# Kernel tuning notes

Measured on AMD Instinct MI355X. Metric: run time of the kernel, lower is better.

## Reference

```python
import jax, jax.numpy as jnp
import numpy as np

H = 8          # num_heads
D = 64         # out_dims = input_dims / num_heads
DM = H * D     # input_dims = 512
B, S = 2, 2048


def _linear(x, W, b):
    # torch nn.Linear: x @ W.T + b, W: [out, in]
    return jnp.einsum('...d,ed->...e', x, W) + b


def setup_inputs() -> dict:
    key = jax.random.key(0)
    ks = jax.random.split(key, 12)
    inp = {
        'query': jax.random.normal(ks[0], (B, S, DM), dtype=jnp.float32),
        'key': jax.random.normal(ks[1], (B, S, DM), dtype=jnp.float32),
        'value': jax.random.normal(ks[2], (B, S, DM), dtype=jnp.float32),
        'Wq': jax.random.normal(ks[3], (D, D), dtype=jnp.float32) * 0.02,
        'bq': jnp.zeros((D,), dtype=jnp.float32),
        'Wk': jax.random.normal(ks[4], (D, D), dtype=jnp.float32) * 0.02,
        'bk': jnp.zeros((D,), dtype=jnp.float32),
        'Wv': jax.random.normal(ks[5], (D, D), dtype=jnp.float32) * 0.02,
        'bv': jnp.zeros((D,), dtype=jnp.float32),
        'Wo': jax.random.normal(ks[6], (DM, DM), dtype=jnp.float32) * 0.02,
        'bo': jnp.zeros((DM,), dtype=jnp.float32),
        'mask': jax.random.randint(ks[7], (B, 1, 1, S), 0, 2, dtype=jnp.int32),
    }
    return inp


def reference(query, key, value, Wq, bq, Wk, bk, Wv, bv, Wo, bo, mask):
    b, qlen = query.shape[0], query.shape[1]
    klen = key.shape[1]
    # split heads: [B, S, H, D]
    q = _linear(query.reshape(b, qlen, H, D), Wq, bq)
    k = _linear(key.reshape(b, klen, H, D), Wk, bk)
    v = _linear(value.reshape(b, klen, H, D), Wv, bv)
    # scores: [B, H, Q, K]
    attn = jnp.einsum('bqhd,bkhd->bhqk', q, k)
    attn = jnp.where(mask == 0, jnp.float32(-1e20), attn)
    # NOTE: original scale is num_heads ** 1 / 2 == H / 2 (Python precedence quirk)
    score = jax.nn.softmax(attn * (2.0 / H), axis=-1)
    # out einsum gives [B, Q, D, H]; flattening gives (d, h) feature order
    out = jnp.einsum('bhqv,bvhd->bqdh', score, v)
    out = out.reshape(b, qlen, D * H)
    return _linear(out, Wo, bo)
```

## Files before the change

### kernel.cpp

```cpp
#include <hip/hip_runtime.h>
#include <math.h>

typedef float f32x4 __attribute__((ext_vector_type(4)));
typedef short s16x8 __attribute__((ext_vector_type(8)));
typedef unsigned short ushort_t;

namespace {
constexpr int kH  = 8;
constexpr int kD  = 64;
constexpr int kDM = 512;
constexpr int kB  = 2;
constexpr int kS  = 2048;
constexpr size_t kNE = (size_t)kB * kH * kS * kD;
}

__device__ __forceinline__ void split_bf16(float x, ushort_t& hi, ushort_t& lo) {
  union { float f; unsigned u; } a; a.f = x;
  hi = (ushort_t)(a.u >> 16);
  union { unsigned u; float f; } hh; hh.u = a.u & 0xffff0000u;
  union { float f; unsigned u; } r; r.f = x - hh.f;
  lo = (ushort_t)(r.u >> 16);
}

__global__ __launch_bounds__(256)
void w_split_kernel(const float* __restrict__ Wo, const float* __restrict__ Wq,
                    const float* __restrict__ Wk, const float* __restrict__ Wv,
                    ushort_t* __restrict__ wo_h, ushort_t* __restrict__ wo_l,
                    ushort_t* __restrict__ wq_h, ushort_t* __restrict__ wq_l,
                    ushort_t* __restrict__ wk_h, ushort_t* __restrict__ wk_l,
                    ushort_t* __restrict__ wv_h, ushort_t* __restrict__ wv_l) {
  const int bid = blockIdx.x;
  if (bid < 256) {
    const int i = (bid * 256 + threadIdx.x) * 4;
    const float4 v = *(const float4*)&Wo[i];
    const int e = i >> 9;
    const float vv[4] = {v.x, v.y, v.z, v.w};
    #pragma unroll
    for (int j = 0; j < 4; ++j) {
      const int f = (i & 511) + j;
      const int g = (f & 7) * 64 + (f >> 3);
      ushort_t hi, lo;
      split_bf16(vv[j], hi, lo);
      wo_h[(size_t)e * kDM + g] = hi;
      wo_l[(size_t)e * kDM + g] = lo;
    }
  } else {
    const int which = bid - 256;
    const float* W = (which == 0) ? Wq : (which == 1) ? Wk : Wv;
    ushort_t* oh = (which == 0) ? wq_h : (which == 1) ? wk_h : wv_h;
    ushort_t* ol = (which == 0) ? wq_l : (which == 1) ? wk_l : wv_l;
    #pragma unroll
    for (int cc = 0; cc < 4; ++cc) {
      const int i = (cc * 256 + threadIdx.x) * 4;
      const float4 v = *(const float4*)&W[i];
      ushort_t h[4], l[4];
      split_bf16(v.x, h[0], l[0]);
      split_bf16(v.y, h[1], l[1]);
      split_bf16(v.z, h[2], l[2]);
      split_bf16(v.w, h[3], l[3]);
      int2 hp, lp;
      hp.x = (int)((unsigned)h[0] | ((unsigned)h[1] << 16));
      hp.y = (int)((unsigned)h[2] | ((unsigned)h[3] << 16));
      lp.x = (int)((unsigned)l[0] | ((unsigned)l[1] << 16));
      lp.y = (int)((unsigned)l[2] | ((unsigned)l[3] << 16));
      *(int2*)&oh[i] = hp;
      *(int2*)&ol[i] = lp;
    }
  }
}

__global__ __launch_bounds__(256, 2)
void kv_proj_kernel(const float* __restrict__ xk, const float* __restrict__ xv,
                    const ushort_t* __restrict__ wk_h, const ushort_t* __restrict__ wk_l,
                    const float* __restrict__ bk,
                    const ushort_t* __restrict__ wv_h, const ushort_t* __restrict__ wv_l,
                    const float* __restrict__ bv,
                    ushort_t* __restrict__ k_hi,
                    ushort_t* __restrict__ vt_hi, ushort_t* __restrict__ vt_lo) {
  __shared__ __align__(16) ushort_t Xh[64][72];
  __shared__ __align__(16) ushort_t Xl[64][72];
  const int which = blockIdx.z;
  const float* x = which ? xv : xk;
  const ushort_t* wh = which ? wv_h : wk_h;
  const ushort_t* wl = which ? wv_l : wk_l;
  const float* bias = which ? bv : bk;
  const int h = blockIdx.y;
  const int t0g = blockIdx.x * 64;
  const int b = t0g >> 11, s0 = t0g & (kS - 1);
  const int tid  = threadIdx.x;
  const int w    = tid >> 6;
  const int lane = tid & 63;
  const int ln   = lane & 15;
  const int quad = lane >> 4;
  const size_t hb = ((size_t)b * kH + h) * (size_t)(kS * kD);

  #pragma unroll
  for (int cc = 0; cc < 4; ++cc) {
    const int id = tid + cc * 256;
    const int r = id >> 4, c = id & 15;
    const float4 v = *(const float4*)&x[((size_t)t0g + r) * kDM + h * kD + c * 4];
    ushort_t hh[4], ll[4];
    split_bf16(v.x, hh[0], ll[0]);
    split_bf16(v.y, hh[1], ll[1]);
    split_bf16(v.z, hh[2], ll[2]);
    split_bf16(v.w, hh[3], ll[3]);
    int2 hp, lp;
    hp.x = (int)((unsigned)hh[0] | ((unsigned)hh[1] << 16));
    hp.y = (int)((unsigned)hh[2] | ((unsigned)hh[3] << 16));
    lp.x = (int)((unsigned)ll[0] | ((unsigned)ll[1] << 16));
    lp.y = (int)((unsigned)ll[2] | ((unsigned)ll[3] << 16));
    *(int2*)&Xh[r][c * 4] = hp;
    *(int2*)&Xl[r][c * 4] = lp;
  }
  __syncthreads();

  f32x4 C[4];
  #pragma unroll
  for (int eb = 0; eb < 4; ++eb) C[eb] = (f32x4){0.f, 0.f, 0.f, 0.f};
  #pragma unroll
  for (int kc = 0; kc < 2; ++kc) {
    const s16x8 ah = *(const s16x8*)&Xh[w * 16 + ln][kc * 32 + quad * 8];
    const s16x8 al = *(const s16x8*)&Xl[w * 16 + ln][kc * 32 + quad * 8];
    s16x8 bh[4], bl[4];
    #pragma unroll
    for (int eb = 0; eb < 4; ++eb) {
      bh[eb] = *(const s16x8*)&wh[(size_t)(eb * 16 + ln) * kD + kc * 32 + quad * 8];
      bl[eb] = *(const s16x8*)&wl[(size_t)(eb * 16 + ln) * kD + kc * 32 + quad * 8];
    }
    #pragma unroll
    for (int eb = 0; eb < 4; ++eb)
      C[eb] = __builtin_amdgcn_mfma_f32_16x16x32_bf16(ah, bh[eb], C[eb], 0, 0, 0);
    #pragma unroll
    for (int eb = 0; eb < 4; ++eb)
      C[eb] = __builtin_amdgcn_mfma_f32_16x16x32_bf16(ah, bl[eb], C[eb], 0, 0, 0);
    #pragma unroll
    for (int eb = 0; eb < 4; ++eb)
      C[eb] = __builtin_amdgcn_mfma_f32_16x16x32_bf16(al, bh[eb], C[eb], 0, 0, 0);
  }
  __syncthreads();

  if (which == 0) {
    #pragma unroll
    for (int eb = 0; eb < 4; ++eb) {
      const float be = bias[eb * 16 + ln];
      #pragma unroll
      for (int r = 0; r < 4; ++r) {
        ushort_t hi, lo;
        split_bf16(C[eb][r] + be, hi, lo);
        Xh[w * 16 + quad * 4 + r][eb * 16 + ln] = hi;
      }
    }
    __syncthreads();
    #pragma unroll
    for (int cc = 0; cc < 2; ++cc) {
      const int id = tid + cc * 256;
      const int r = id >> 3, c = id & 7;
      *(int4*)&k_hi[hb + (size_t)(s0 + r) * kD + c * 8] = *(int4*)&Xh[r][c * 8];
    }
  } else {
    #pragma unroll
    for (int eb = 0; eb < 4; ++eb) {
      const float be = bias[eb * 16 + ln];
      #pragma unroll
      for (int r = 0; r < 4; ++r) {
        ushort_t hi, lo;
        split_bf16(C[eb][r] + be, hi, lo);
        Xh[eb * 16 + ln][w * 16 + quad * 4 + r] = hi;
        Xl[eb * 16 + ln][w * 16 + quad * 4 + r] = lo;
      }
    }
    __syncthreads();
    #pragma unroll
    for (int cc = 0; cc < 2; ++cc) {
      const int id = tid + cc * 256;
      const int r = id >> 3, c = id & 7;
      *(int4*)&vt_hi[hb + (size_t)r * kS + s0 + c * 8] = *(int4*)&Xh[r][c * 8];
      *(int4*)&vt_lo[hb + (size_t)r * kS + s0 + c * 8] = *(int4*)&Xl[r][c * 8];
    }
  }
}

__global__ __launch_bounds__(256, 2)
void attn_kernel(const float* __restrict__ xq,
                 const ushort_t* __restrict__ wq_h, const ushort_t* __restrict__ wq_l,
                 const float* __restrict__ bq,
                 const ushort_t* __restrict__ k_hi,
                 const ushort_t* __restrict__ vt_hi, const ushort_t* __restrict__ vt_lo,
                 const int* __restrict__ mask,
                 ushort_t* __restrict__ ctx_h, ushort_t* __restrict__ ctx_l) {
  __shared__ __align__(16) ushort_t Kh[64][72];
  __shared__ __align__(16) ushort_t Vh[64][72];
  __shared__ __align__(16) ushort_t Vl[64][72];
  __shared__ __align__(16) unsigned P32[4][16][68];
  __shared__ float Mz[64];

  const int tid  = threadIdx.x;
  const int w    = tid >> 6;
  const int lane = tid & 63;
  const int ln   = lane & 15;
  const int quad = lane >> 4;
  const int h = blockIdx.y, b = blockIdx.z;
  const int q0 = blockIdx.x * 64;
  const size_t hb = ((size_t)b * kH + h) * (size_t)(kS * kD);

  #pragma unroll
  for (int cc = 0; cc < 4; ++cc) {
    const int id = tid + cc * 256;
    const int r = id >> 4, c = id & 15;
    const float4 v =
        *(const float4*)&xq[((size_t)b * kS + q0 + r) * kDM + h * kD + c * 4];
    ushort_t hh[4], ll[4];
    split_bf16(v.x, hh[0], ll[0]);
    split_bf16(v.y, hh[1], ll[1]);
    split_bf16(v.z, hh[2], ll[2]);
    split_bf16(v.w, hh[3], ll[3]);
    int2 hp, lp;
    hp.x = (int)((unsigned)hh[0] | ((unsigned)hh[1] << 16));
    hp.y = (int)((unsigned)hh[2] | ((unsigned)hh[3] << 16));
    lp.x = (int)((unsigned)ll[0] | ((unsigned)ll[1] << 16));
    lp.y = (int)((unsigned)ll[2] | ((unsigned)ll[3] << 16));
    *(int2*)&Kh[r][c * 4] = hp;
    *(int2*)&Vh[r][c * 4] = lp;
  }
  __syncthreads();
  {
    f32x4 C[4];
    #pragma unroll
    for (int eb = 0; eb < 4; ++eb) C[eb] = (f32x4){0.f, 0.f, 0.f, 0.f};
    #pragma unroll
    for (int kc = 0; kc < 2; ++kc) {
      const s16x8 ah = *(const s16x8*)&Kh[w * 16 + ln][kc * 32 + quad * 8];
      const s16x8 al = *(const s16x8*)&Vh[w * 16 + ln][kc * 32 + quad * 8];
      s16x8 bh[4], bl[4];
      #pragma unroll
      for (int eb = 0; eb < 4; ++eb) {
        bh[eb] = *(const s16x8*)&wq_h[(size_t)(eb * 16 + ln) * kD + kc * 32 + quad * 8];
        bl[eb] = *(const s16x8*)&wq_l[(size_t)(eb * 16 + ln) * kD + kc * 32 + quad * 8];
      }
      #pragma unroll
      for (int eb = 0; eb < 4; ++eb)
        C[eb] = __builtin_amdgcn_mfma_f32_16x16x32_bf16(ah, bh[eb], C[eb], 0, 0, 0);
      #pragma unroll
      for (int eb = 0; eb < 4; ++eb)
        C[eb] = __builtin_amdgcn_mfma_f32_16x16x32_bf16(ah, bl[eb], C[eb], 0, 0, 0);
      #pragma unroll
      for (int eb = 0; eb < 4; ++eb)
        C[eb] = __builtin_amdgcn_mfma_f32_16x16x32_bf16(al, bh[eb], C[eb], 0, 0, 0);
    }
    __syncthreads();
    #pragma unroll
    for (int eb = 0; eb < 4; ++eb) {
      const float be = bq[eb * 16 + ln];
      #pragma unroll
      for (int r = 0; r < 4; ++r) {
        ushort_t hi, lo;
        split_bf16(C[eb][r] + be, hi, lo);
        Kh[w * 16 + quad * 4 + r][eb * 16 + ln] = hi;
        Vh[w * 16 + quad * 4 + r][eb * 16 + ln] = lo;
      }
    }
    __syncthreads();
  }
  s16x8 aqh[2], aql[2];
  #pragma unroll
  for (int db = 0; db < 2; ++db) {
    aqh[db] = *(const s16x8*)&Kh[w * 16 + ln][db * 32 + quad * 8];
    aql[db] = *(const s16x8*)&Vh[w * 16 + ln][db * 32 + quad * 8];
  }

  f32x4 O[4];
  #pragma unroll
  for (int db = 0; db < 4; ++db) O[db] = (f32x4){0.f, 0.f, 0.f, 0.f};
  float rs[4] = {0.f, 0.f, 0.f, 0.f};

  for (int kt = 0; kt < kS / 64; ++kt) {
    __syncthreads();
    {
      const ushort_t* gkh = k_hi + hb + (size_t)kt * 64 * kD;
      const ushort_t* gvh = vt_hi + hb + (size_t)kt * 64;
      const ushort_t* gvl = vt_lo + hb + (size_t)kt * 64;
      #pragma unroll
      for (int cc = 0; cc < 2; ++cc) {
        const int c = tid + cc * 256;
        const int r = c >> 3, off = (c & 7) * 8;
        *(int4*)&Kh[r][off] = *(const int4*)&gkh[r * kD + off];
        *(int4*)&Vh[r][off] = *(const int4*)&gvh[(size_t)r * kS + off];
        *(int4*)&Vl[r][off] = *(const int4*)&gvl[(size_t)r * kS + off];
      }
      if (tid < 64) Mz[tid] = (mask[(size_t)b * kS + kt * 64 + tid] != 0) ? 1.0f : 0.0f;
    }
    __syncthreads();

    f32x4 C[4];
    #pragma unroll
    for (int kb = 0; kb < 4; ++kb) C[kb] = (f32x4){0.f, 0.f, 0.f, 0.f};
    #pragma unroll
    for (int db = 0; db < 2; ++db) {
      s16x8 bh[4];
      #pragma unroll
      for (int kb = 0; kb < 4; ++kb)
        bh[kb] = *(const s16x8*)&Kh[kb * 16 + ln][db * 32 + quad * 8];
      #pragma unroll
      for (int kb = 0; kb < 4; ++kb)
        C[kb] = __builtin_amdgcn_mfma_f32_16x16x32_bf16(aqh[db], bh[kb], C[kb], 0, 0, 0);
      #pragma unroll
      for (int kb = 0; kb < 4; ++kb)
        C[kb] = __builtin_amdgcn_mfma_f32_16x16x32_bf16(aql[db], bh[kb], C[kb], 0, 0, 0);
    }

    #pragma unroll
    for (int kb = 0; kb < 4; ++kb) {
      const float mz = Mz[kb * 16 + ln];
      #pragma unroll
      for (int r = 0; r < 4; ++r) {
        const float p = mz * __expf(0.25f * C[kb][r]);
        rs[r] += p;
        ushort_t hi, lo;
        split_bf16(p, hi, lo);
        P32[w][quad * 4 + r][kb * 16 + ln] = ((unsigned)hi << 16) | (unsigned)lo;
      }
    }

    #pragma unroll
    for (int kh = 0; kh < 2; ++kh) {
      const int4 u0 = *(const int4*)&P32[w][ln][kh * 32 + quad * 8];
      const int4 u1 = *(const int4*)&P32[w][ln][kh * 32 + quad * 8 + 4];
      const unsigned uu[8] = {(unsigned)u0.x, (unsigned)u0.y, (unsigned)u0.z, (unsigned)u0.w,
                              (unsigned)u1.x, (unsigned)u1.y, (unsigned)u1.z, (unsigned)u1.w};
      s16x8 ph, pl;
      #pragma unroll
      for (int j = 0; j < 8; ++j) {
        ph[j] = (short)(uu[j] >> 16);
        pl[j] = (short)(uu[j] & 0xffffu);
      }
      s16x8 vh[4], vl[4];
      #pragma unroll
      for (int db = 0; db < 4; ++db) {
        vh[db] = *(const s16x8*)&Vh[db * 16 + ln][kh * 32 + quad * 8];
        vl[db] = *(const s16x8*)&Vl[db * 16 + ln][kh * 32 + quad * 8];
      }
      #pragma unroll
      for (int db = 0; db < 4; ++db)
        O[db] = __builtin_amdgcn_mfma_f32_16x16x32_bf16(ph, vh[db], O[db], 0, 0, 0);
      #pragma unroll
      for (int db = 0; db < 4; ++db)
        O[db] = __builtin_amdgcn_mfma_f32_16x16x32_bf16(ph, vl[db], O[db], 0, 0, 0);
      #pragma unroll
      for (int db = 0; db < 4; ++db)
        O[db] = __builtin_amdgcn_mfma_f32_16x16x32_bf16(pl, vh[db], O[db], 0, 0, 0);
    }
  }

  #pragma unroll
  for (int m = 1; m < 16; m <<= 1) {
    #pragma unroll
    for (int r = 0; r < 4; ++r) rs[r] += __shfl_xor(rs[r], m);
  }
  float inv[4];
  #pragma unroll
  for (int r = 0; r < 4; ++r) inv[r] = 1.0f / rs[r];

  __syncthreads();
  #pragma unroll
  for (int db = 0; db < 4; ++db) {
    #pragma unroll
    for (int r = 0; r < 4; ++r) {
      ushort_t hi, lo;
      split_bf16(O[db][r] * inv[r], hi, lo);
      Kh[w * 16 + quad * 4 + r][db * 16 + ln] = hi;
      Vh[w * 16 + quad * 4 + r][db * 16 + ln] = lo;
    }
  }
  __syncthreads();
  #pragma unroll
  for (int cc = 0; cc < 2; ++cc) {
    const int id = tid + cc * 256;
    const int r = id >> 3, c = id & 7;
    const size_t o = ((size_t)b * kS + q0 + r) * kDM + h * kD + c * 8;
    *(int4*)&ctx_h[o] = *(int4*)&Kh[r][c * 8];
    *(int4*)&ctx_l[o] = *(int4*)&Vh[r][c * 8];
  }
}

__global__ __launch_bounds__(256, 2)
void out_proj_kernel(const ushort_t* __restrict__ ch, const ushort_t* __restrict__ cl,
                     const ushort_t* __restrict__ wh, const ushort_t* __restrict__ wl,
                     const float* __restrict__ bo, float* __restrict__ out) {
  __shared__ __align__(16) ushort_t Ah[64][72];
  __shared__ __align__(16) ushort_t Al[64][72];
  __shared__ __align__(16) ushort_t Bh[64][72];
  __shared__ __align__(16) ushort_t Bl[64][72];
  const int t0 = blockIdx.x * 64;
  const int e0 = blockIdx.y * 64;
  const int tid  = threadIdx.x;
  const int w    = tid >> 6;
  const int lane = tid & 63;
  const int ln   = lane & 15;
  const int quad = lane >> 4;

  f32x4 C[4];
  #pragma unroll
  for (int eb = 0; eb < 4; ++eb) C[eb] = (f32x4){0.f, 0.f, 0.f, 0.f};

  for (int k0 = 0; k0 < kDM; k0 += 64) {
    __syncthreads();
    #pragma unroll
    for (int cc = 0; cc < 2; ++cc) {
      const int c = tid + cc * 256;
      const int r = c >> 3, off = (c & 7) * 8;
      *(int4*)&Ah[r][off] = *(const int4*)&ch[(size_t)(t0 + r) * kDM + k0 + off];
      *(int4*)&Al[r][off] = *(const int4*)&cl[(size_t)(t0 + r) * kDM + k0 + off];
      *(int4*)&Bh[r][off] = *(const int4*)&wh[(size_t)(e0 + r) * kDM + k0 + off];
      *(int4*)&Bl[r][off] = *(const int4*)&wl[(size_t)(e0 + r) * kDM + k0 + off];
    }
    __syncthreads();
    #pragma unroll
    for (int kc = 0; kc < 2; ++kc) {
      const s16x8 ah = *(const s16x8*)&Ah[w * 16 + ln][kc * 32 + quad * 8];
      const s16x8 al = *(const s16x8*)&Al[w * 16 + ln][kc * 32 + quad * 8];
      s16x8 bh[4], bl[4];
      #pragma unroll
      for (int eb = 0; eb < 4; ++eb) {
        bh[eb] = *(const s16x8*)&Bh[eb * 16 + ln][kc * 32 + quad * 8];
        bl[eb] = *(const s16x8*)&Bl[eb * 16 + ln][kc * 32 + quad * 8];
      }
      #pragma unroll
      for (int eb = 0; eb < 4; ++eb)
        C[eb] = __builtin_amdgcn_mfma_f32_16x16x32_bf16(ah, bh[eb], C[eb], 0, 0, 0);
      #pragma unroll
      for (int eb = 0; eb < 4; ++eb)
        C[eb] = __builtin_amdgcn_mfma_f32_16x16x32_bf16(ah, bl[eb], C[eb], 0, 0, 0);
      #pragma unroll
      for (int eb = 0; eb < 4; ++eb)
        C[eb] = __builtin_amdgcn_mfma_f32_16x16x32_bf16(al, bh[eb], C[eb], 0, 0, 0);
    }
  }

  #pragma unroll
  for (int eb = 0; eb < 4; ++eb) {
    const int e = e0 + eb * 16 + ln;
    const float be = bo[e];
    #pragma unroll
    for (int r = 0; r < 4; ++r) {
      const int t = t0 + w * 16 + quad * 4 + r;
      out[(size_t)t * kDM + e] = C[eb][r] + be;
    }
  }
}

extern "C" void kernel_launch(void* const* d_in, const int* in_sizes, int n_in,
                              void* d_out, int out_size, void* d_ws, size_t ws_size,
                              hipStream_t stream) {
  const float* query = (const float*)d_in[0];
  const float* key   = (const float*)d_in[1];
  const float* value = (const float*)d_in[2];
  const float* Wq = (const float*)d_in[3];
  const float* bq = (const float*)d_in[4];
  const float* Wk = (const float*)d_in[5];
  const float* bk = (const float*)d_in[6];
  const float* Wv = (const float*)d_in[7];
  const float* bv = (const float*)d_in[8];
  const float* Wo = (const float*)d_in[9];
  const float* bo = (const float*)d_in[10];
  const int* mask = (const int*)d_in[11];
  float* out = (float*)d_out;

  ushort_t* k_hi  = (ushort_t*)d_ws;
  ushort_t* vt_hi = k_hi + kNE;
  ushort_t* vt_lo = vt_hi + kNE;
  ushort_t* ctx_h = vt_lo + kNE;
  ushort_t* ctx_l = ctx_h + kNE;
  ushort_t* wo_h  = ctx_l + kNE;
  ushort_t* wo_l  = wo_h + (size_t)kDM * kDM;
  ushort_t* wq_h  = wo_l + (size_t)kDM * kDM;
  ushort_t* wq_l  = wq_h + kD * kD;
  ushort_t* wk_h  = wq_l + kD * kD;
  ushort_t* wk_l  = wk_h + kD * kD;
  ushort_t* wv_h  = wk_l + kD * kD;
  ushort_t* wv_l  = wv_h + kD * kD;

  w_split_kernel<<<dim3(259), 256, 0, stream>>>(
      Wo, Wq, Wk, Wv, wo_h, wo_l, wq_h, wq_l, wk_h, wk_l, wv_h, wv_l);
  kv_proj_kernel<<<dim3(kB * kS / 64, kH, 2), 256, 0, stream>>>(
      key, value, wk_h, wk_l, bk, wv_h, wv_l, bv, k_hi, vt_hi, vt_lo);
  attn_kernel<<<dim3(kS / 64, kH, kB), 256, 0, stream>>>(
      query, wq_h, wq_l, bq, k_hi, vt_hi, vt_lo, mask, ctx_h, ctx_l);
  out_proj_kernel<<<dim3(kB * kS / 64, kDM / 64), 256, 0, stream>>>(
      ctx_h, ctx_l, wo_h, wo_l, bo, out);
}
```

Baseline: 183.6 us.

## Split attention key range across two blocks and merge with combine kernel

Each attention block now processes half of the key sequence, doubling the grid from 512 to 1024 blocks, and writes unnormalized partial outputs plus row sums to workspace. A new combine kernel adds the two halves, normalizes, and re-splits into bf16 hi/lo for the output projection. The inner loop is restructured into 32-key sub-tiles with a smaller P buffer, and launch bounds are raised to 4 blocks per CU to raise occupancy. The extra kernel launch and partial-output traffic are the cost. The split is safe without a max because no max subtraction is used.

```diff
diff --git a/kernel.cpp b/kernel.cpp
--- a/kernel.cpp
+++ b/kernel.cpp
@@ -11,7 +11,8 @@
 constexpr int kDM = 512;
 constexpr int kB  = 2;
 constexpr int kS  = 2048;
-constexpr size_t kNE = (size_t)kB * kH * kS * kD;
+constexpr size_t kNE = (size_t)kB * kS * kDM;
+constexpr size_t kNL = (size_t)kB * kH * kS;
 }
 
 __device__ __forceinline__ void split_bf16(float x, ushort_t& hi, ushort_t& lo) {
@@ -20,6 +21,12 @@
   union { unsigned u; float f; } hh; hh.u = a.u & 0xffff0000u;
   union { float f; unsigned u; } r; r.f = x - hh.f;
   lo = (ushort_t)(r.u >> 16);
+}
+__device__ __forceinline__ float unp_hi(unsigned u) {
+  union { unsigned u; float f; } a; a.u = u & 0xffff0000u; return a.f;
+}
+__device__ __forceinline__ float unp_lo(unsigned u) {
+  union { unsigned u; float f; } a; a.u = u << 16; return a.f;
 }
 
 __global__ __launch_bounds__(256)
@@ -180,18 +187,18 @@
   }
 }
 
-__global__ __launch_bounds__(256, 2)
+__global__ __launch_bounds__(256, 4)
 void attn_kernel(const float* __restrict__ xq,
                  const ushort_t* __restrict__ wq_h, const ushort_t* __restrict__ wq_l,
                  const float* __restrict__ bq,
                  const ushort_t* __restrict__ k_hi,
                  const ushort_t* __restrict__ vt_hi, const ushort_t* __restrict__ vt_lo,
                  const int* __restrict__ mask,
-                 ushort_t* __restrict__ ctx_h, ushort_t* __restrict__ ctx_l) {
+                 unsigned* __restrict__ Opk, float* __restrict__ lws) {
   __shared__ __align__(16) ushort_t Kh[64][72];
   __shared__ __align__(16) ushort_t Vh[64][72];
   __shared__ __align__(16) ushort_t Vl[64][72];
-  __shared__ __align__(16) unsigned P32[4][16][68];
+  __shared__ __align__(16) unsigned Pbuf[4][16][36];
   __shared__ float Mz[64];
 
   const int tid  = threadIdx.x;
@@ -199,8 +206,10 @@
   const int lane = tid & 63;
   const int ln   = lane & 15;
   const int quad = lane >> 4;
-  const int h = blockIdx.y, b = blockIdx.z;
-  const int q0 = blockIdx.x * 64;
+  const int h    = blockIdx.y;
+  const int b    = blockIdx.z >> 1;
+  const int half = blockIdx.z & 1;
+  const int q0   = blockIdx.x * 64;
   const size_t hb = ((size_t)b * kH + h) * (size_t)(kS * kD);
 
   #pragma unroll
@@ -273,7 +282,8 @@
   for (int db = 0; db < 4; ++db) O[db] = (f32x4){0.f, 0.f, 0.f, 0.f};
   float rs[4] = {0.f, 0.f, 0.f, 0.f};
 
-  for (int kt = 0; kt < kS / 64; ++kt) {
+  const int kt0 = half * 16;
+  for (int kt = kt0; kt < kt0 + 16; ++kt) {
     __syncthreads();
     {
       const ushort_t* gkh = k_hi + hb + (size_t)kt * 64 * kD;
@@ -291,63 +301,58 @@
     }
     __syncthreads();
 
-    f32x4 C[4];
-    #pragma unroll
-    for (int kb = 0; kb < 4; ++kb) C[kb] = (f32x4){0.f, 0.f, 0.f, 0.f};
-    #pragma unroll
-    for (int db = 0; db < 2; ++db) {
-      s16x8 bh[4];
-      #pragma unroll
-      for (int kb = 0; kb < 4; ++kb)
-        bh[kb] = *(const s16x8*)&Kh[kb * 16 + ln][db * 32 + quad * 8];
-      #pragma unroll
-      for (int kb = 0; kb < 4; ++kb)
-        C[kb] = __builtin_amdgcn_mfma_f32_16x16x32_bf16(aqh[db], bh[kb], C[kb], 0, 0, 0);
-      #pragma unroll
-      for (int kb = 0; kb < 4; ++kb)
-        C[kb] = __builtin_amdgcn_mfma_f32_16x16x32_bf16(aql[db], bh[kb], C[kb], 0, 0, 0);
-    }
-
-    #pragma unroll
-    for (int kb = 0; kb < 4; ++kb) {
-      const float mz = Mz[kb * 16 + ln];
-      #pragma unroll
-      for (int r = 0; r < 4; ++r) {
-        const float p = mz * __expf(0.25f * C[kb][r]);
-        rs[r] += p;
-        ushort_t hi, lo;
-        split_bf16(p, hi, lo);
-        P32[w][quad * 4 + r][kb * 16 + ln] = ((unsigned)hi << 16) | (unsigned)lo;
-      }
-    }
-
-    #pragma unroll
-    for (int kh = 0; kh < 2; ++kh) {
-      const int4 u0 = *(const int4*)&P32[w][ln][kh * 32 + quad * 8];
-      const int4 u1 = *(const int4*)&P32[w][ln][kh * 32 + quad * 8 + 4];
-      const unsigned uu[8] = {(unsigned)u0.x, (unsigned)u0.y, (unsigned)u0.z, (unsigned)u0.w,
-                              (unsigned)u1.x, (unsigned)u1.y, (unsigned)u1.z, (unsigned)u1.w};
-      s16x8 ph, pl;
-      #pragma unroll
-      for (int j = 0; j < 8; ++j) {
-        ph[j] = (short)(uu[j] >> 16);
-        pl[j] = (short)(uu[j] & 0xffffu);
-      }
-      s16x8 vh[4], vl[4];
-      #pragma unroll
-      for (int db = 0; db < 4; ++db) {
-        vh[db] = *(const s16x8*)&Vh[db * 16 + ln][kh * 32 + quad * 8];
-        vl[db] = *(const s16x8*)&Vl[db * 16 + ln][kh * 32 + quad * 8];
-      }
-      #pragma unroll
-      for (int db = 0; db < 4; ++db)
-        O[db] = __builtin_amdgcn_mfma_f32_16x16x32_bf16(ph, vh[db], O[db], 0, 0, 0);
-      #pragma unroll
-      for (int db = 0; db < 4; ++db)
-        O[db] = __builtin_amdgcn_mfma_f32_16x16x32_bf16(ph, vl[db], O[db], 0, 0, 0);
-      #pragma unroll
-      for (int db = 0; db < 4; ++db)
-        O[db] = __builtin_amdgcn_mfma_f32_16x16x32_bf16(pl, vh[db], O[db], 0, 0, 0);
+    #pragma unroll
+    for (int h32 = 0; h32 < 2; ++h32) {
+      f32x4 C[2];
+      C[0] = (f32x4){0.f, 0.f, 0.f, 0.f};
+      C[1] = (f32x4){0.f, 0.f, 0.f, 0.f};
+      #pragma unroll
+      for (int db = 0; db < 2; ++db) {
+        s16x8 bh0 = *(const s16x8*)&Kh[h32 * 32 + ln][db * 32 + quad * 8];
+        s16x8 bh1 = *(const s16x8*)&Kh[h32 * 32 + 16 + ln][db * 32 + quad * 8];
+        C[0] = __builtin_amdgcn_mfma_f32_16x16x32_bf16(aqh[db], bh0, C[0], 0, 0, 0);
+        C[1] = __builtin_amdgcn_mfma_f32_16x16x32_bf16(aqh[db], bh1, C[1], 0, 0, 0);
+        C[0] = __builtin_amdgcn_mfma_f32_16x16x32_bf16(aql[db], bh0, C[0], 0, 0, 0);
+        C[1] = __builtin_amdgcn_mfma_f32_16x16x32_bf16(aql[db], bh1, C[1], 0, 0, 0);
+      }
+      #pragma unroll
+      for (int kb = 0; kb < 2; ++kb) {
+        const float mz = Mz[h32 * 32 + kb * 16 + ln];
+        #pragma unroll
+        for (int r = 0; r < 4; ++r) {
+          const float p = mz * __expf(0.25f * C[kb][r]);
+          rs[r] += p;
+          ushort_t hi, lo;
+          split_bf16(p, hi, lo);
+          Pbuf[w][quad * 4 + r][kb * 16 + ln] = ((unsigned)hi << 16) | (unsigned)lo;
+        }
+      }
+      {
+        const uint4 u0 = *(const uint4*)&Pbuf[w][ln][quad * 8];
+        const uint4 u1 = *(const uint4*)&Pbuf[w][ln][quad * 8 + 4];
+        const unsigned uu[8] = {u0.x, u0.y, u0.z, u0.w, u1.x, u1.y, u1.z, u1.w};
+        s16x8 ph, pl;
+        #pragma unroll
+        for (int j = 0; j < 8; ++j) {
+          ph[j] = (short)(uu[j] >> 16);
+          pl[j] = (short)(uu[j] & 0xffffu);
+        }
+        s16x8 vh[4], vl[4];
+        #pragma unroll
+        for (int db = 0; db < 4; ++db) {
+          vh[db] = *(const s16x8*)&Vh[db * 16 + ln][h32 * 32 + quad * 8];
+          vl[db] = *(const s16x8*)&Vl[db * 16 + ln][h32 * 32 + quad * 8];
+        }
+        #pragma unroll
+        for (int db = 0; db < 4; ++db)
+          O[db] = __builtin_amdgcn_mfma_f32_16x16x32_bf16(ph, vh[db], O[db], 0, 0, 0);
+        #pragma unroll
+        for (int db = 0; db < 4; ++db)
+          O[db] = __builtin_amdgcn_mfma_f32_16x16x32_bf16(ph, vl[db], O[db], 0, 0, 0);
+        #pragma unroll
+        for (int db = 0; db < 4; ++db)
+          O[db] = __builtin_amdgcn_mfma_f32_16x16x32_bf16(pl, vh[db], O[db], 0, 0, 0);
+      }
     }
   }
 
@@ -356,30 +361,61 @@
     #pragma unroll
     for (int r = 0; r < 4; ++r) rs[r] += __shfl_xor(rs[r], m);
   }
-  float inv[4];
-  #pragma unroll
-  for (int r = 0; r < 4; ++r) inv[r] = 1.0f / rs[r];
-
-  __syncthreads();
+  if (ln == 0) {
+    float* lp = lws + (size_t)half * kNL + ((size_t)b * kH + h) * kS +
+                q0 + w * 16 + quad * 4;
+    #pragma unroll
+    for (int r = 0; r < 4; ++r) lp[r] = rs[r];
+  }
+
+  unsigned* op = Opk + (size_t)half * kNE;
+  const size_t obase = ((size_t)b * kS + q0 + w * 16 + quad * 4) * kDM + h * kD;
   #pragma unroll
   for (int db = 0; db < 4; ++db) {
     #pragma unroll
     for (int r = 0; r < 4; ++r) {
       ushort_t hi, lo;
-      split_bf16(O[db][r] * inv[r], hi, lo);
-      Kh[w * 16 + quad * 4 + r][db * 16 + ln] = hi;
-      Vh[w * 16 + quad * 4 + r][db * 16 + ln] = lo;
-    }
-  }
-  __syncthreads();
-  #pragma unroll
-  for (int cc = 0; cc < 2; ++cc) {
-    const int id = tid + cc * 256;
-    const int r = id >> 3, c = id & 7;
-    const size_t o = ((size_t)b * kS + q0 + r) * kDM + h * kD + c * 8;
-    *(int4*)&ctx_h[o] = *(int4*)&Kh[r][c * 8];
-    *(int4*)&ctx_l[o] = *(int4*)&Vh[r][c * 8];
-  }
+      split_bf16(O[db][r], hi, lo);
+      op[obase + (size_t)r * kDM + db * 16 + ln] = ((unsigned)hi << 16) | (unsigned)lo;
+    }
+  }
+}
+
+__global__ __launch_bounds__(256)
+void combine_kernel(const unsigned* __restrict__ Opk, const float* __restrict__ lws,
+                    ushort_t* __restrict__ ctx_h, ushort_t* __restrict__ ctx_l) {
+  const size_t base = ((size_t)blockIdx.x * 256 + threadIdx.x) * 8;
+  const int t = (int)(base >> 9);
+  const int f0 = (int)(base & 511);
+  const int hh = f0 >> 6;
+  const int b = t >> 11, s = t & (kS - 1);
+  const size_t li = ((size_t)b * kH + hh) * kS + s;
+  const float linv = 1.0f / (lws[li] + lws[kNL + li]);
+
+  const uint4 a0 = *(const uint4*)&Opk[base];
+  const uint4 a1 = *(const uint4*)&Opk[base + 4];
+  const uint4 c0 = *(const uint4*)&Opk[kNE + base];
+  const uint4 c1 = *(const uint4*)&Opk[kNE + base + 4];
+  const unsigned ua[8] = {a0.x, a0.y, a0.z, a0.w, a1.x, a1.y, a1.z, a1.w};
+  const unsigned uc[8] = {c0.x, c0.y, c0.z, c0.w, c1.x, c1.y, c1.z, c1.w};
+  ushort_t hi[8], lo[8];
+  #pragma unroll
+  for (int j = 0; j < 8; ++j) {
+    const float o = (unp_hi(ua[j]) + unp_lo(ua[j])) +
+                    (unp_hi(uc[j]) + unp_lo(uc[j]));
+    split_bf16(o * linv, hi[j], lo[j]);
+  }
+  int4 hp, lp;
+  hp.x = (int)((unsigned)hi[0] | ((unsigned)hi[1] << 16));
+  hp.y = (int)((unsigned)hi[2] | ((unsigned)hi[3] << 16));
+  hp.z = (int)((unsigned)hi[4] | ((unsigned)hi[5] << 16));
+  hp.w = (int)((unsigned)hi[6] | ((unsigned)hi[7] << 16));
+  lp.x = (int)((unsigned)lo[0] | ((unsigned)lo[1] << 16));
+  lp.y = (int)((unsigned)lo[2] | ((unsigned)lo[3] << 16));
+  lp.z = (int)((unsigned)lo[4] | ((unsigned)lo[5] << 16));
+  lp.w = (int)((unsigned)lo[6] | ((unsigned)lo[7] << 16));
+  *(int4*)&ctx_h[base] = hp;
+  *(int4*)&ctx_l[base] = lp;
 }
 
 __global__ __launch_bounds__(256, 2)
@@ -468,23 +504,27 @@
   ushort_t* k_hi  = (ushort_t*)d_ws;
   ushort_t* vt_hi = k_hi + kNE;
   ushort_t* vt_lo = vt_hi + kNE;
-  ushort_t* ctx_h = vt_lo + kNE;
-  ushort_t* ctx_l = ctx_h + kNE;
-  ushort_t* wo_h  = ctx_l + kNE;
+  ushort_t* wo_h  = vt_lo + kNE;
   ushort_t* wo_l  = wo_h + (size_t)kDM * kDM;
-  ushort_t* wq_h  = wo_l + (size_t)kDM * kDM;
+  unsigned* Opk   = (unsigned*)(wo_l + (size_t)kDM * kDM);
+  float*    lws   = (float*)(Opk + 2 * kNE);
+  ushort_t* wq_h  = (ushort_t*)(lws + 2 * kNL);
   ushort_t* wq_l  = wq_h + kD * kD;
   ushort_t* wk_h  = wq_l + kD * kD;
   ushort_t* wk_l  = wk_h + kD * kD;
   ushort_t* wv_h  = wk_l + kD * kD;
   ushort_t* wv_l  = wv_h + kD * kD;
+  ushort_t* ctx_h = k_hi;
+  ushort_t* ctx_l = vt_hi;
 
   w_split_kernel<<<dim3(259), 256, 0, stream>>>(
       Wo, Wq, Wk, Wv, wo_h, wo_l, wq_h, wq_l, wk_h, wk_l, wv_h, wv_l);
   kv_proj_kernel<<<dim3(kB * kS / 64, kH, 2), 256, 0, stream>>>(
       key, value, wk_h, wk_l, bk, wv_h, wv_l, bv, k_hi, vt_hi, vt_lo);
-  attn_kernel<<<dim3(kS / 64, kH, kB), 256, 0, stream>>>(
-      query, wq_h, wq_l, bq, k_hi, vt_hi, vt_lo, mask, ctx_h, ctx_l);
+  attn_kernel<<<dim3(kS / 64, kH, kB * 2), 256, 0, stream>>>(
+      query, wq_h, wq_l, bq, k_hi, vt_hi, vt_lo, mask, Opk, lws);
+  combine_kernel<<<dim3((unsigned)(kNE / 8 / 256)), 256, 0, stream>>>(
+      Opk, lws, ctx_h, ctx_l);
   out_proj_kernel<<<dim3(kB * kS / 64, kDM / 64), 256, 0, stream>>>(
       ctx_h, ctx_l, wo_h, wo_l, bo, out);
 }
```

New measurement: 182.6 us. No clear change (-0.5%).

## Split attention over key quarters with atomic accumulation and drop low-precision V/P terms

Applied to the files above, without the earlier changes.

The attention kernel now splits the key dimension into four chunks per block and runs 512-thread blocks covering 128 queries. Partial unnormalised outputs and row sums are accumulated with float atomics into a zeroed workspace, and normalisation moves into the output projection. V and P drop their low bf16 halves (V stored round-to-nearest bf16, P rounded), so the PV step needs one MFMA pass instead of three and V needs one less load stream. This adds parallelism and cuts MFMA work, at the cost of a memset, atomic traffic, and reduced precision in the PV product.

```diff
diff --git a/kernel.cpp b/kernel.cpp
--- a/kernel.cpp
+++ b/kernel.cpp
@@ -11,7 +11,8 @@
 constexpr int kDM = 512;
 constexpr int kB  = 2;
 constexpr int kS  = 2048;
-constexpr size_t kNE = (size_t)kB * kH * kS * kD;
+constexpr size_t kNE = (size_t)kB * kS * kDM;
+constexpr size_t kNL = (size_t)kB * kH * kS;
 }
 
 __device__ __forceinline__ void split_bf16(float x, ushort_t& hi, ushort_t& lo) {
@@ -20,6 +21,11 @@
   union { unsigned u; float f; } hh; hh.u = a.u & 0xffff0000u;
   union { float f; unsigned u; } r; r.f = x - hh.f;
   lo = (ushort_t)(r.u >> 16);
+}
+__device__ __forceinline__ ushort_t rne_bf16(float x) {
+  union { float f; unsigned u; } a; a.f = x;
+  const unsigned t = a.u + 0x7fffu + ((a.u >> 16) & 1u);
+  return (ushort_t)(t >> 16);
 }
 
 __global__ __launch_bounds__(256)
@@ -75,8 +81,7 @@
                     const float* __restrict__ bk,
                     const ushort_t* __restrict__ wv_h, const ushort_t* __restrict__ wv_l,
                     const float* __restrict__ bv,
-                    ushort_t* __restrict__ k_hi,
-                    ushort_t* __restrict__ vt_hi, ushort_t* __restrict__ vt_lo) {
+                    ushort_t* __restrict__ k_hi, ushort_t* __restrict__ vt_hi) {
   __shared__ __align__(16) ushort_t Xh[64][72];
   __shared__ __align__(16) ushort_t Xl[64][72];
   const int which = blockIdx.z;
@@ -144,11 +149,8 @@
     for (int eb = 0; eb < 4; ++eb) {
       const float be = bias[eb * 16 + ln];
       #pragma unroll
-      for (int r = 0; r < 4; ++r) {
-        ushort_t hi, lo;
-        split_bf16(C[eb][r] + be, hi, lo);
-        Xh[w * 16 + quad * 4 + r][eb * 16 + ln] = hi;
-      }
+      for (int r = 0; r < 4; ++r)
+        Xh[w * 16 + quad * 4 + r][eb * 16 + ln] = rne_bf16(C[eb][r] + be);
     }
     __syncthreads();
     #pragma unroll
@@ -162,12 +164,8 @@
     for (int eb = 0; eb < 4; ++eb) {
       const float be = bias[eb * 16 + ln];
       #pragma unroll
-      for (int r = 0; r < 4; ++r) {
-        ushort_t hi, lo;
-        split_bf16(C[eb][r] + be, hi, lo);
-        Xh[eb * 16 + ln][w * 16 + quad * 4 + r] = hi;
-        Xl[eb * 16 + ln][w * 16 + quad * 4 + r] = lo;
-      }
+      for (int r = 0; r < 4; ++r)
+        Xh[eb * 16 + ln][w * 16 + quad * 4 + r] = rne_bf16(C[eb][r] + be);
     }
     __syncthreads();
     #pragma unroll
@@ -175,62 +173,54 @@
       const int id = tid + cc * 256;
       const int r = id >> 3, c = id & 7;
       *(int4*)&vt_hi[hb + (size_t)r * kS + s0 + c * 8] = *(int4*)&Xh[r][c * 8];
-      *(int4*)&vt_lo[hb + (size_t)r * kS + s0 + c * 8] = *(int4*)&Xl[r][c * 8];
-    }
-  }
-}
-
-__global__ __launch_bounds__(256, 2)
+    }
+  }
+}
+
+__global__ __launch_bounds__(512, 6)
 void attn_kernel(const float* __restrict__ xq,
                  const ushort_t* __restrict__ wq_h, const ushort_t* __restrict__ wq_l,
                  const float* __restrict__ bq,
-                 const ushort_t* __restrict__ k_hi,
-                 const ushort_t* __restrict__ vt_hi, const ushort_t* __restrict__ vt_lo,
+                 const ushort_t* __restrict__ k_hi, const ushort_t* __restrict__ vt_hi,
                  const int* __restrict__ mask,
-                 ushort_t* __restrict__ ctx_h, ushort_t* __restrict__ ctx_l) {
-  __shared__ __align__(16) ushort_t Kh[64][72];
-  __shared__ __align__(16) ushort_t Vh[64][72];
-  __shared__ __align__(16) ushort_t Vl[64][72];
-  __shared__ __align__(16) unsigned P32[4][16][68];
+                 float* __restrict__ O32, float* __restrict__ lws) {
+  __shared__ __align__(16) unsigned char smem[34816];
   __shared__ float Mz[64];
+  ushort_t (*Kh)[72] = (ushort_t(*)[72])smem;
+  ushort_t (*Vh)[72] = (ushort_t(*)[72])(smem + 9216);
+  ushort_t (*Pb)[16][40] = (ushort_t(*)[16][40])(smem + 18432);
+  unsigned (*QT)[68] = (unsigned(*)[68])smem;
 
   const int tid  = threadIdx.x;
   const int w    = tid >> 6;
   const int lane = tid & 63;
   const int ln   = lane & 15;
   const int quad = lane >> 4;
-  const int h = blockIdx.y, b = blockIdx.z;
-  const int q0 = blockIdx.x * 64;
+  const int h    = blockIdx.y;
+  const int b    = blockIdx.z >> 2;
+  const int quarter = blockIdx.z & 3;
+  const int q0   = blockIdx.x * 128;
   const size_t hb = ((size_t)b * kH + h) * (size_t)(kS * kD);
 
-  #pragma unroll
-  for (int cc = 0; cc < 4; ++cc) {
-    const int id = tid + cc * 256;
-    const int r = id >> 4, c = id & 15;
-    const float4 v =
-        *(const float4*)&xq[((size_t)b * kS + q0 + r) * kDM + h * kD + c * 4];
-    ushort_t hh[4], ll[4];
-    split_bf16(v.x, hh[0], ll[0]);
-    split_bf16(v.y, hh[1], ll[1]);
-    split_bf16(v.z, hh[2], ll[2]);
-    split_bf16(v.w, hh[3], ll[3]);
-    int2 hp, lp;
-    hp.x = (int)((unsigned)hh[0] | ((unsigned)hh[1] << 16));
-    hp.y = (int)((unsigned)hh[2] | ((unsigned)hh[3] << 16));
-    lp.x = (int)((unsigned)ll[0] | ((unsigned)ll[1] << 16));
-    lp.y = (int)((unsigned)ll[2] | ((unsigned)ll[3] << 16));
-    *(int2*)&Kh[r][c * 4] = hp;
-    *(int2*)&Vh[r][c * 4] = lp;
-  }
-  __syncthreads();
+  s16x8 aqh[2], aql[2];
   {
+    const int qrow = q0 + w * 16 + ln;
     f32x4 C[4];
     #pragma unroll
     for (int eb = 0; eb < 4; ++eb) C[eb] = (f32x4){0.f, 0.f, 0.f, 0.f};
     #pragma unroll
     for (int kc = 0; kc < 2; ++kc) {
-      const s16x8 ah = *(const s16x8*)&Kh[w * 16 + ln][kc * 32 + quad * 8];
-      const s16x8 al = *(const s16x8*)&Vh[w * 16 + ln][kc * 32 + quad * 8];
+      const float* xp = &xq[((size_t)b * kS + qrow) * kDM + h * kD + kc * 32 + quad * 8];
+      const float4 x0 = *(const float4*)xp;
+      const float4 x1 = *(const float4*)(xp + 4);
+      const float xs[8] = {x0.x, x0.y, x0.z, x0.w, x1.x, x1.y, x1.z, x1.w};
+      s16x8 ah, al;
+      #pragma unroll
+      for (int j = 0; j < 8; ++j) {
+        ushort_t hi, lo;
+        split_bf16(xs[j], hi, lo);
+        ah[j] = (short)hi; al[j] = (short)lo;
+      }
       s16x8 bh[4], bl[4];
       #pragma unroll
       for (int eb = 0; eb < 4; ++eb) {
@@ -247,7 +237,6 @@
       for (int eb = 0; eb < 4; ++eb)
         C[eb] = __builtin_amdgcn_mfma_f32_16x16x32_bf16(al, bh[eb], C[eb], 0, 0, 0);
     }
-    __syncthreads();
     #pragma unroll
     for (int eb = 0; eb < 4; ++eb) {
       const float be = bq[eb * 16 + ln];
@@ -255,99 +244,78 @@
       for (int r = 0; r < 4; ++r) {
         ushort_t hi, lo;
         split_bf16(C[eb][r] + be, hi, lo);
-        Kh[w * 16 + quad * 4 + r][eb * 16 + ln] = hi;
-        Vh[w * 16 + quad * 4 + r][eb * 16 + ln] = lo;
-      }
-    }
-    __syncthreads();
-  }
-  s16x8 aqh[2], aql[2];
-  #pragma unroll
-  for (int db = 0; db < 2; ++db) {
-    aqh[db] = *(const s16x8*)&Kh[w * 16 + ln][db * 32 + quad * 8];
-    aql[db] = *(const s16x8*)&Vh[w * 16 + ln][db * 32 + quad * 8];
-  }
+        QT[w * 16 + quad * 4 + r][eb * 16 + ln] = ((unsigned)hi << 16) | (unsigned)lo;
+      }
+    }
+    #pragma unroll
+    for (int db = 0; db < 2; ++db) {
+      const uint4 u0 = *(const uint4*)&QT[w * 16 + ln][db * 32 + quad * 8];
+      const uint4 u1 = *(const uint4*)&QT[w * 16 + ln][db * 32 + quad * 8 + 4];
+      const unsigned uu[8] = {u0.x, u0.y, u0.z, u0.w, u1.x, u1.y, u1.z, u1.w};
+      #pragma unroll
+      for (int j = 0; j < 8; ++j) {
+        aqh[db][j] = (short)(uu[j] >> 16);
+        aql[db][j] = (short)(uu[j] & 0xffffu);
+      }
+    }
+  }
+  __syncthreads();
 
   f32x4 O[4];
   #pragma unroll
   for (int db = 0; db < 4; ++db) O[db] = (f32x4){0.f, 0.f, 0.f, 0.f};
   float rs[4] = {0.f, 0.f, 0.f, 0.f};
 
-  for (int kt = 0; kt < kS / 64; ++kt) {
+  const int kt0 = quarter * 8;
+  for (int kt = kt0; kt < kt0 + 8; ++kt) {
     __syncthreads();
     {
       const ushort_t* gkh = k_hi + hb + (size_t)kt * 64 * kD;
       const ushort_t* gvh = vt_hi + hb + (size_t)kt * 64;
-      const ushort_t* gvl = vt_lo + hb + (size_t)kt * 64;
-      #pragma unroll
-      for (int cc = 0; cc < 2; ++cc) {
-        const int c = tid + cc * 256;
-        const int r = c >> 3, off = (c & 7) * 8;
-        *(int4*)&Kh[r][off] = *(const int4*)&gkh[r * kD + off];
-        *(int4*)&Vh[r][off] = *(const int4*)&gvh[(size_t)r * kS + off];
-        *(int4*)&Vl[r][off] = *(const int4*)&gvl[(size_t)r * kS + off];
-      }
+      const int r = tid >> 3, c = tid & 7;
+      *(int4*)&Kh[r][c * 8] = *(const int4*)&gkh[r * kD + c * 8];
+      *(int4*)&Vh[r][c * 8] = *(const int4*)&gvh[(size_t)r * kS + c * 8];
       if (tid < 64) Mz[tid] = (mask[(size_t)b * kS + kt * 64 + tid] != 0) ? 1.0f : 0.0f;
     }
     __syncthreads();
 
-    f32x4 C[4];
-    #pragma unroll
-    for (int kb = 0; kb < 4; ++kb) C[kb] = (f32x4){0.f, 0.f, 0.f, 0.f};
-    #pragma unroll
-    for (int db = 0; db < 2; ++db) {
-      s16x8 bh[4];
-      #pragma unroll
-      for (int kb = 0; kb < 4; ++kb)
-        bh[kb] = *(const s16x8*)&Kh[kb * 16 + ln][db * 32 + quad * 8];
-      #pragma unroll
-      for (int kb = 0; kb < 4; ++kb)
-        C[kb] = __builtin_amdgcn_mfma_f32_16x16x32_bf16(aqh[db], bh[kb], C[kb], 0, 0, 0);
-      #pragma unroll
-      for (int kb = 0; kb < 4; ++kb)
-        C[kb] = __builtin_amdgcn_mfma_f32_16x16x32_bf16(aql[db], bh[kb], C[kb], 0, 0, 0);
-    }
-
-    #pragma unroll
-    for (int kb = 0; kb < 4; ++kb) {
-      const float mz = Mz[kb * 16 + ln];
-      #pragma unroll
-      for (int r = 0; r < 4; ++r) {
-        const float p = mz * __expf(0.25f * C[kb][r]);
-        rs[r] += p;
-        ushort_t hi, lo;
-        split_bf16(p, hi, lo);
-        P32[w][quad * 4 + r][kb * 16 + ln] = ((unsigned)hi << 16) | (unsigned)lo;
-      }
-    }
-
-    #pragma unroll
-    for (int kh = 0; kh < 2; ++kh) {
-      const int4 u0 = *(const int4*)&P32[w][ln][kh * 32 + quad * 8];
-      const int4 u1 = *(const int4*)&P32[w][ln][kh * 32 + quad * 8 + 4];
-      const unsigned uu[8] = {(unsigned)u0.x, (unsigned)u0.y, (unsigned)u0.z, (unsigned)u0.w,
-                              (unsigned)u1.x, (unsigned)u1.y, (unsigned)u1.z, (unsigned)u1.w};
-      s16x8 ph, pl;
-      #pragma unroll
-      for (int j = 0; j < 8; ++j) {
-        ph[j] = (short)(uu[j] >> 16);
-        pl[j] = (short)(uu[j] & 0xffffu);
-      }
-      s16x8 vh[4], vl[4];
-      #pragma unroll
-      for (int db = 0; db < 4; ++db) {
-        vh[db] = *(const s16x8*)&Vh[db * 16 + ln][kh * 32 + quad * 8];
-        vl[db] = *(const s16x8*)&Vl[db * 16 + ln][kh * 32 + quad * 8];
-      }
-      #pragma unroll
-      for (int db = 0; db < 4; ++db)
-        O[db] = __builtin_amdgcn_mfma_f32_16x16x32_bf16(ph, vh[db], O[db], 0, 0, 0);
-      #pragma unroll
-      for (int db = 0; db < 4; ++db)
-        O[db] = __builtin_amdgcn_mfma_f32_16x16x32_bf16(ph, vl[db], O[db], 0, 0, 0);
-      #pragma unroll
-      for (int db = 0; db < 4; ++db)
-        O[db] = __builtin_amdgcn_mfma_f32_16x16x32_bf16(pl, vh[db], O[db], 0, 0, 0);
+    #pragma unroll
+    for (int h32 = 0; h32 < 2; ++h32) {
+      f32x4 C[2];
+      C[0] = (f32x4){0.f, 0.f, 0.f, 0.f};
+      C[1] = (f32x4){0.f, 0.f, 0.f, 0.f};
+      #pragma unroll
+      for (int db = 0; db < 2; ++db) {
+        const s16x8 bh0 = *(const s16x8*)&Kh[h32 * 32 + ln][db * 32 + quad * 8];
+        const s16x8 bh1 = *(const s16x8*)&Kh[h32 * 32 + 16 + ln][db * 32 + quad * 8];
+        C[0] = __builtin_amdgcn_mfma_f32_16x16x32_bf16(aqh[db], bh0, C[0], 0, 0, 0);
+        C[1] = __builtin_amdgcn_mfma_f32_16x16x32_bf16(aqh[db], bh1, C[1], 0, 0, 0);
+        C[0] = __builtin_amdgcn_mfma_f32_16x16x32_bf16(aql[db], bh0, C[0], 0, 0, 0);
+        C[1] = __builtin_amdgcn_mfma_f32_16x16x32_bf16(aql[db], bh1, C[1], 0, 0, 0);
+      }
+      #pragma unroll
+      for (int kb = 0; kb < 2; ++kb) {
+        const float mz = Mz[h32 * 32 + kb * 16 + ln];
+        #pragma unroll
+        for (int r = 0; r < 4; ++r) {
+          const float p = mz * __expf(0.25f * C[kb][r]);
+          union { float f; unsigned u; } pa; pa.f = p;
+          const unsigned t = pa.u + 0x7fffu + ((pa.u >> 16) & 1u);
+          Pb[w][quad * 4 + r][kb * 16 + ln] = (ushort_t)(t >> 16);
+          union { unsigned u; float f; } pr; pr.u = t & 0xffff0000u;
+          rs[r] += pr.f;
+        }
+      }
+      {
+        const s16x8 ph = *(const s16x8*)&Pb[w][ln][quad * 8];
+        s16x8 vh[4];
+        #pragma unroll
+        for (int db = 0; db < 4; ++db)
+          vh[db] = *(const s16x8*)&Vh[db * 16 + ln][h32 * 32 + quad * 8];
+        #pragma unroll
+        for (int db = 0; db < 4; ++db)
+          O[db] = __builtin_amdgcn_mfma_f32_16x16x32_bf16(ph, vh[db], O[db], 0, 0, 0);
+      }
     }
   }
 
@@ -356,60 +324,75 @@
     #pragma unroll
     for (int r = 0; r < 4; ++r) rs[r] += __shfl_xor(rs[r], m);
   }
-  float inv[4];
-  #pragma unroll
-  for (int r = 0; r < 4; ++r) inv[r] = 1.0f / rs[r];
-
-  __syncthreads();
+  if (ln == 0) {
+    float* lp = lws + ((size_t)b * kH + h) * kS + q0 + w * 16 + quad * 4;
+    #pragma unroll
+    for (int r = 0; r < 4; ++r) atomicAdd(&lp[r], rs[r]);
+  }
+  const size_t obase = ((size_t)b * kS + q0 + w * 16 + quad * 4) * kDM + h * kD;
   #pragma unroll
   for (int db = 0; db < 4; ++db) {
     #pragma unroll
-    for (int r = 0; r < 4; ++r) {
-      ushort_t hi, lo;
-      split_bf16(O[db][r] * inv[r], hi, lo);
-      Kh[w * 16 + quad * 4 + r][db * 16 + ln] = hi;
-      Vh[w * 16 + quad * 4 + r][db * 16 + ln] = lo;
-    }
-  }
-  __syncthreads();
-  #pragma unroll
-  for (int cc = 0; cc < 2; ++cc) {
-    const int id = tid + cc * 256;
-    const int r = id >> 3, c = id & 7;
-    const size_t o = ((size_t)b * kS + q0 + r) * kDM + h * kD + c * 8;
-    *(int4*)&ctx_h[o] = *(int4*)&Kh[r][c * 8];
-    *(int4*)&ctx_l[o] = *(int4*)&Vh[r][c * 8];
+    for (int r = 0; r < 4; ++r)
+      atomicAdd(&O32[obase + (size_t)r * kDM + db * 16 + ln], O[db][r]);
   }
 }
 
 __global__ __launch_bounds__(256, 2)
-void out_proj_kernel(const ushort_t* __restrict__ ch, const ushort_t* __restrict__ cl,
+void out_proj_kernel(const float* __restrict__ O32, const float* __restrict__ lws,
                      const ushort_t* __restrict__ wh, const ushort_t* __restrict__ wl,
                      const float* __restrict__ bo, float* __restrict__ out) {
   __shared__ __align__(16) ushort_t Ah[64][72];
   __shared__ __align__(16) ushort_t Al[64][72];
   __shared__ __align__(16) ushort_t Bh[64][72];
   __shared__ __align__(16) ushort_t Bl[64][72];
+  __shared__ float linv[kH][64];
   const int t0 = blockIdx.x * 64;
   const int e0 = blockIdx.y * 64;
+  const int b  = t0 >> 11;
+  const int s0 = t0 & (kS - 1);
   const int tid  = threadIdx.x;
   const int w    = tid >> 6;
   const int lane = tid & 63;
   const int ln   = lane & 15;
   const int quad = lane >> 4;
 
+  for (int id = tid; id < kH * 64; id += 256) {
+    const int hh = id >> 6, r = id & 63;
+    linv[hh][r] = 1.0f / lws[((size_t)b * kH + hh) * kS + s0 + r];
+  }
+
   f32x4 C[4];
   #pragma unroll
   for (int eb = 0; eb < 4; ++eb) C[eb] = (f32x4){0.f, 0.f, 0.f, 0.f};
 
   for (int k0 = 0; k0 < kDM; k0 += 64) {
     __syncthreads();
+    const int hh = k0 >> 6;
+    #pragma unroll
+    for (int cc = 0; cc < 4; ++cc) {
+      const int id = tid + cc * 256;
+      const int r = id >> 4, c4 = id & 15;
+      float4 v = *(const float4*)&O32[(size_t)(t0 + r) * kDM + k0 + c4 * 4];
+      const float li = linv[hh][r];
+      v.x *= li; v.y *= li; v.z *= li; v.w *= li;
+      ushort_t h4[4], l4[4];
+      split_bf16(v.x, h4[0], l4[0]);
+      split_bf16(v.y, h4[1], l4[1]);
+      split_bf16(v.z, h4[2], l4[2]);
+      split_bf16(v.w, h4[3], l4[3]);
+      int2 hp, lp;
+      hp.x = (int)((unsigned)h4[0] | ((unsigned)h4[1] << 16));
+      hp.y = (int)((unsigned)h4[2] | ((unsigned)h4[3] << 16));
+      lp.x = (int)((unsigned)l4[0] | ((unsigned)l4[1] << 16));
+      lp.y = (int)((unsigned)l4[2] | ((unsigned)l4[3] << 16));
+      *(int2*)&Ah[r][c4 * 4] = hp;
+      *(int2*)&Al[r][c4 * 4] = lp;
+    }
     #pragma unroll
     for (int cc = 0; cc < 2; ++cc) {
-      const int c = tid + cc * 256;
-      const int r = c >> 3, off = (c & 7) * 8;
-      *(int4*)&Ah[r][off] = *(const int4*)&ch[(size_t)(t0 + r) * kDM + k0 + off];
-      *(int4*)&Al[r][off] = *(const int4*)&cl[(size_t)(t0 + r) * kDM + k0 + off];
+      const int id = tid + cc * 256;
+      const int r = id >> 3, off = (id & 7) * 8;
       *(int4*)&Bh[r][off] = *(const int4*)&wh[(size_t)(e0 + r) * kDM + k0 + off];
       *(int4*)&Bl[r][off] = *(const int4*)&wl[(size_t)(e0 + r) * kDM + k0 + off];
     }
@@ -467,24 +450,24 @@
 
   ushort_t* k_hi  = (ushort_t*)d_ws;
   ushort_t* vt_hi = k_hi + kNE;
-  ushort_t* vt_lo = vt_hi + kNE;
-  ushort_t* ctx_h = vt_lo + kNE;
-  ushort_t* ctx_l = ctx_h + kNE;
-  ushort_t* wo_h  = ctx_l + kNE;
+  ushort_t* wo_h  = vt_hi + kNE;
   ushort_t* wo_l  = wo_h + (size_t)kDM * kDM;
-  ushort_t* wq_h  = wo_l + (size_t)kDM * kDM;
+  float*    O32   = (float*)(wo_l + (size_t)kDM * kDM);
+  float*    lws   = O32 + kNE;
+  ushort_t* wq_h  = (ushort_t*)(lws + kNL);
   ushort_t* wq_l  = wq_h + kD * kD;
   ushort_t* wk_h  = wq_l + kD * kD;
   ushort_t* wk_l  = wk_h + kD * kD;
   ushort_t* wv_h  = wk_l + kD * kD;
   ushort_t* wv_l  = wv_h + kD * kD;
 
+  hipMemsetAsync(O32, 0, (kNE + kNL) * sizeof(float), stream);
   w_split_kernel<<<dim3(259), 256, 0, stream>>>(
       Wo, Wq, Wk, Wv, wo_h, wo_l, wq_h, wq_l, wk_h, wk_l, wv_h, wv_l);
   kv_proj_kernel<<<dim3(kB * kS / 64, kH, 2), 256, 0, stream>>>(
-      key, value, wk_h, wk_l, bk, wv_h, wv_l, bv, k_hi, vt_hi, vt_lo);
-  attn_kernel<<<dim3(kS / 64, kH, kB), 256, 0, stream>>>(
-      query, wq_h, wq_l, bq, k_hi, vt_hi, vt_lo, mask, ctx_h, ctx_l);
+      key, value, wk_h, wk_l, bk, wv_h, wv_l, bv, k_hi, vt_hi);
+  attn_kernel<<<dim3(kS / 128, kH, kB * 4), 512, 0, stream>>>(
+      query, wq_h, wq_l, bq, k_hi, vt_hi, mask, O32, lws);
   out_proj_kernel<<<dim3(kB * kS / 64, kDM / 64), 256, 0, stream>>>(
-      ctx_h, ctx_l, wo_h, wo_l, bo, out);
-}
+      O32, lws, wo_h, wo_l, bo, out);
+}
```

After: 186.4 us. No clear change (+1.5%).
